# Kernel tuning notes

Hardware: AMD Instinct MI355X
Metric: run time of the kernel (lower is better)

## Reference

```python
import jax, jax.numpy as jnp
import numpy as np

HEADS = 16
SEGS = 8


def _rotate_half(x):
    x1, x2 = jnp.split(x, 2, axis=-1)
    return jnp.concatenate([-x2, x1], axis=-1)


def _split_heads(t, h):
    b, n, dim = t.shape
    d = dim // h
    return t.reshape(b, n, h, d).transpose(0, 2, 1, 3).reshape(b * h, n, d)


def _merge_heads(t, b, h):
    c, n, d = t.shape
    return t.reshape(b, h, n, d).transpose(0, 2, 1, 3).reshape(b, n, h * d)


def setup_inputs() -> dict:
    key = jax.random.key(0)
    ks = jax.random.split(key, 5)
    b, n, dim = 2, 4096, 1024
    x = jax.random.normal(ks[0], (b, n, dim), dtype=jnp.float32)
    w = lambda k: jax.random.normal(k, (dim, dim), dtype=jnp.float32) * 0.02
    return {
        'x': x,
        'Wq': w(ks[1]),
        'Wkv': w(ks[2]),
        'Wo': w(ks[3]),
        'bo': jnp.zeros((dim,), jnp.float32),
        'Wo0': w(ks[4]),
        'bo0': jnp.zeros((dim,), jnp.float32),
    }


def reference(x, Wq, Wkv, Wo, bo, Wo0, bo0):
    b, n, dim = x.shape
    h = HEADS
    d = dim // h
    s = SEGS
    m = n // s  # segment_len
    mask_value = -jnp.finfo(x.dtype).max

    q = _split_heads(x @ Wq, h)    # (b*h, n, d)
    kv = _split_heads(x @ Wkv, h)  # (b*h, n, d)  (serves as both keys and values)

    # rotary embedding (layer_num == 0 branch)
    inv_freq = 1.0 / (10000.0 ** (jnp.arange(0, d, 2, dtype=jnp.float32) / d))
    freqs = jnp.arange(n, dtype=jnp.float32)[:, None] * inv_freq[None, :]  # (n, d/2)
    rot = jnp.concatenate([freqs, freqs], axis=-1)[None]  # (1, n, d)
    cos, sin = jnp.cos(rot), jnp.sin(rot)
    q = q * cos + _rotate_half(q) * sin
    kv = kv * cos + _rotate_half(kv) * sin

    q = q * (d ** -0.5)

    qs = q.reshape(-1, s, m, d)   # (c, s, m, d)
    kvs = kv.reshape(-1, s, m, d)

    # overlapping windows: segment t paired with segment t+1 as kv context
    kvs_ccs = jnp.concatenate([kvs[:, :-1], kvs[:, 1:]], axis=2)  # (c, s-1, 2m, d)
    qs_ccs = qs[:, 1:]                                            # (c, s-1, m, d)

    # NOTE: original computes lkv = LayerNorm(kvs_ccs) but never uses it (dead code) -> omitted.

    lsim = jnp.einsum('csmd,csnd->csmn', qs_ccs, kvs_ccs)  # (c, s-1, m, 2m)
    causal = jnp.triu(jnp.ones((m, m), dtype=bool), 1)
    # causal mask only applied to second half of keys (the own segment t+1)
    lsim = jnp.concatenate(
        [lsim[..., :m], jnp.where(causal, mask_value, lsim[..., m:])], axis=-1)

    attn0 = jnp.einsum('csmd,csnd->csmn', qs[:, :1], kvs[:, :1])  # (c, 1, m, m)
    attn0 = jnp.where(causal, mask_value, attn0)

    attn0 = jax.nn.softmax(attn0, axis=-1)
    attn1 = jax.nn.softmax(lsim, axis=-1)

    out0 = jnp.einsum('csij,csjd->csid', attn0, kvs[:, :1]).reshape(-1, m, d)
    out1 = jnp.einsum('csij,csjd->csid', attn1, kvs_ccs).reshape(-1, (s - 1) * m, d)

    out0 = _merge_heads(out0, b, h) @ Wo0 + bo0  # (b, m, dim)
    out1 = _merge_heads(out1, b, h) @ Wo + bo    # (b, (s-1)*m, dim)
    return jnp.concatenate([out0, out1], axis=1)  # (b, n, dim)
```

## Files before the change

kernel.cpp:

```cpp
#include <hip/hip_runtime.h>
#include <hip/hip_bf16.h>
#include <float.h>

using bf16 = __hip_bfloat16;
typedef __attribute__((ext_vector_type(8))) short bf16x8;
typedef __attribute__((ext_vector_type(4))) float f32x4;
typedef __attribute__((ext_vector_type(16))) float f32x16;

#define DIM   1024
#define NSEQ  4096
#define BATCH 2
#define NH    16
#define HD    64
#define NSEG  8
#define MSEG  512
#define ROWS  (BATCH*NSEQ)
#define NC    (BATCH*NH)
#define QSCALE (0.125f * 1.44269504f)

__device__ __forceinline__ float fast_exp2(float x) {
    float r;
    asm volatile("v_exp_f32 %0, %1" : "=v"(r) : "v"(x));
    return r;
}

__device__ __forceinline__ void gload16(const bf16* g, bf16* l) {
    __builtin_amdgcn_global_load_lds((const __attribute__((address_space(1))) unsigned int*)g,
                                     (__attribute__((address_space(3))) unsigned int*)l, 16, 0, 0);
}

__global__ void k_prep(const float* __restrict__ x, bf16* __restrict__ Xb,
                       const float* __restrict__ Wq, const float* __restrict__ Wkv,
                       const float* __restrict__ Wo, const float* __restrict__ Wo0,
                       bf16* __restrict__ WqT, bf16* __restrict__ WkvT,
                       bf16* __restrict__ WoT, bf16* __restrict__ Wo0T,
                       float* __restrict__ cosT, float* __restrict__ sinT) {
    __shared__ float tile[32][33];
    int b = blockIdx.x, tid = threadIdx.x;
    if (b < 8192) {
        int i = (b * 256 + tid) * 4;
        float4 v = *(const float4*)&x[i];
        union { bf16 h[4]; uint2 u; } p;
        p.h[0] = __float2bfloat16(v.x);
        p.h[1] = __float2bfloat16(v.y);
        p.h[2] = __float2bfloat16(v.z);
        p.h[3] = __float2bfloat16(v.w);
        *(uint2*)&Xb[i] = p.u;
    } else if (b < 12288) {
        int zz = (b - 8192) >> 10;
        int bb = (b - 8192) & 1023;
        int bxt = (bb & 31) * 32, byt = (bb >> 5) * 32;
        const float* W = (zz == 0) ? Wq : (zz == 1) ? Wkv : (zz == 2) ? Wo : Wo0;
        bf16* Wt = (zz == 0) ? WqT : (zz == 1) ? WkvT : (zz == 2) ? WoT : Wo0T;
        int tx = tid & 31, ty = tid >> 5;
        for (int ii = ty; ii < 32; ii += 8)
            tile[ii][tx] = W[(size_t)(byt + ii) * DIM + bxt + tx];
        __syncthreads();
        for (int ii = ty; ii < 32; ii += 8)
            Wt[(size_t)(bxt + ii) * DIM + byt + tx] = __float2bfloat16(tile[tx][ii]);
    } else {
        int idx = (b - 12288) * 256 + tid;
        int t = idx >> 5, ii = idx & 31;
        float freq = 1.0f / powf(10000.0f, (float)(2 * ii) * (1.0f / 64.0f));
        float a = (float)t * freq;
        cosT[idx] = cosf(a);
        sinT[idx] = sinf(a);
    }
}

__launch_bounds__(256, 3)
__global__ void k_gemm_qkv(const bf16* __restrict__ A, const bf16* __restrict__ Bq,
                           const bf16* __restrict__ Bkv, const float* __restrict__ cosT,
                           const float* __restrict__ sinT, bf16* __restrict__ Qb,
                           bf16* __restrict__ KVf) {
    __shared__ alignas(16) bf16 SH[24576];
    bf16* AsB = SH;
    bf16* BsB = SH + 12288;
    const int K = DIM;
    int tid = threadIdx.x;
    int lane = tid & 63, wave = tid >> 6;
    int hi = lane >> 5, lq = lane & 31;
    int wr = (wave >> 1) * 64, wc = (wave & 1) * 64;
    int id = blockIdx.x;
    int xcd = id & 7, rank = id >> 3;
    int by = xcd * 8 + (rank >> 4);
    int bxx = rank & 15;
    int m0 = by * 128;
    bool isQ = (bxx < 8);
    const bf16* Bt = isQ ? Bq : Bkv;
    int n0 = (bxx & 7) * 128;
    int row = lane & 15, kk = (lane >> 4) * 8;
    int kkA = kk ^ (((lane >> 1) & 3) << 3);
    int ch0 = wave * 128 + lane, ch1 = ch0 + 64;
    int r0 = ch0 >> 2, c0e = (ch0 & 3) * 8;
    int r1 = ch1 >> 2, c1e = (ch1 & 3) * 8;
    int c0s = c0e ^ (((r0 >> 1) & 3) << 3);
    int c1s = c1e ^ (((r1 >> 1) & 3) << 3);
    f32x4 acc[4][4] = {};

    auto stage = [&](int k0, int b) {
        gload16(&A[(size_t)(m0 + r0) * K + k0 + c0s], &AsB[b * 4096 + wave * 1024]);
        gload16(&A[(size_t)(m0 + r1) * K + k0 + c1s], &AsB[b * 4096 + wave * 1024 + 512]);
        gload16(&Bt[(size_t)(n0 + r0) * K + k0 + c0s], &BsB[b * 4096 + wave * 1024]);
        gload16(&Bt[(size_t)(n0 + r1) * K + k0 + c1s], &BsB[b * 4096 + wave * 1024 + 512]);
    };
    stage(0, 0);
    stage(32, 1);
    asm volatile("s_waitcnt vmcnt(4)" ::: "memory");
    __builtin_amdgcn_s_barrier();
    __builtin_amdgcn_sched_barrier(0);
    int cur = 0;
    for (int k = 0; k < 32; ++k) {
        if (k + 2 < 32) {
            int nb = cur + 2; if (nb >= 3) nb -= 3;
            stage(k * 32 + 64, nb);
        }
        bf16x8 af[4], bfr[4];
#pragma unroll
        for (int mt = 0; mt < 4; ++mt) af[mt] = *(const bf16x8*)&AsB[cur * 4096 + (wr + mt * 16 + row) * 32 + kkA];
#pragma unroll
        for (int nt = 0; nt < 4; ++nt) bfr[nt] = *(const bf16x8*)&BsB[cur * 4096 + (wc + nt * 16 + row) * 32 + kkA];
#pragma unroll
        for (int mt = 0; mt < 4; ++mt)
#pragma unroll
            for (int nt = 0; nt < 4; ++nt)
                acc[mt][nt] = __builtin_amdgcn_mfma_f32_16x16x32_bf16(af[mt], bfr[nt], acc[mt][nt], 0, 0, 0);
        if (k + 1 < 32) {
            if (k + 2 < 32) asm volatile("s_waitcnt vmcnt(4)" ::: "memory");
            else            asm volatile("s_waitcnt vmcnt(0)" ::: "memory");
            __builtin_amdgcn_s_barrier();
            __builtin_amdgcn_sched_barrier(0);
        }
        cur = cur + 1; if (cur == 3) cur = 0;
    }
    __syncthreads();
    bf16* Tw = SH + wave * (64 * 72);
    int orow = (lane >> 4) * 4, ocol = lane & 15;
    int head_g = (n0 + wc) >> 6;
    float sc = isQ ? QSCALE : 1.0f;
    int bidx = (m0 + wr) >> 12;
    int tbase = (m0 + wr) & (NSEQ - 1);
    int cch = bidx * NH + head_g;
#pragma unroll
    for (int mt = 0; mt < 4; ++mt) {
#pragma unroll
        for (int i = 0; i < 4; ++i) {
            int rl = mt * 16 + orow + i;
            int t = tbase + rl;
#pragma unroll
            for (int nt = 0; nt < 2; ++nt) {
                int e = nt * 16 + ocol;
                float x1 = acc[mt][nt][i], x2 = acc[mt][nt + 2][i];
                float cv = cosT[t * 32 + e], sv = sinT[t * 32 + e];
                Tw[rl * 72 + e]      = __float2bfloat16((x1 * cv - x2 * sv) * sc);
                Tw[rl * 72 + e + 32] = __float2bfloat16((x2 * cv + x1 * sv) * sc);
            }
        }
    }
    if (isQ) {
        int rsub = lane >> 3, dg = (lane & 7) * 8;
        size_t qbase = ((size_t)cch * NSEQ + tbase) * HD;
#pragma unroll
        for (int rr = 0; rr < 8; ++rr) {
            int rl = rr * 8 + rsub;
            *(uint4*)&Qb[qbase + (size_t)rl * HD + dg] = *(const uint4*)&Tw[rl * 72 + dg];
        }
    } else {
        size_t kvfbase = ((size_t)cch * 128 + (tbase >> 5)) * 4096;
#pragma unroll
        for (int st = 0; st < 2; ++st) {
            size_t tb = kvfbase + (size_t)st * 4096;
#pragma unroll
            for (int f = 0; f < 4; ++f)
                *(uint4*)&KVf[tb + f * 512 + lane * 8] =
                    *(const uint4*)&Tw[(st * 32 + lq) * 72 + f * 16 + hi * 8];
#pragma unroll
            for (int m = 0; m < 4; ++m) {
                int d0 = (m >> 1) * 32, sb = m & 1;
                union { bf16 h[8]; uint4 u; } pk;
#pragma unroll
                for (int j = 0; j < 8; ++j)
                    pk.h[j] = Tw[(st * 32 + sb * 16 + hi * 8 + j) * 72 + d0 + lq];
                *(uint4*)&KVf[tb + (size_t)(4 + m) * 512 + lane * 8] = pk.u;
            }
        }
    }
}

__launch_bounds__(256, 4)
__global__ void k_gemm_out(const bf16* __restrict__ A, const bf16* __restrict__ Bt0,
                           const bf16* __restrict__ Bt1, const float* __restrict__ bias0,
                           const float* __restrict__ bias1, float* __restrict__ C) {
    __shared__ alignas(16) bf16 As[3][128 * 32];
    __shared__ alignas(16) bf16 Bs[3][64 * 32];
    const int K = DIM;
    int tid = threadIdx.x;
    int lane = tid & 63, wave = tid >> 6;
    int wr = (wave >> 1) * 64, wc = (wave & 1) * 32;
    int id = blockIdx.x;
    int xcd = id & 7, rank = id >> 3;
    int by = xcd * 8 + (rank >> 4);
    int bx = rank & 15;
    int m0 = by * 128, n0 = bx * 64;
    bool first = (m0 & (NSEQ - 1)) < MSEG;
    const bf16* Bt = first ? Bt0 : Bt1;
    const float* bias = first ? bias0 : bias1;
    int row = lane & 15, kk = (lane >> 4) * 8;
    int kkA = kk ^ (((lane >> 1) & 3) << 3);
    int ch0 = wave * 128 + lane, ch1 = ch0 + 64;
    int r0 = ch0 >> 2, c0e = (ch0 & 3) * 8;
    int r1 = ch1 >> 2, c1e = (ch1 & 3) * 8;
    int c0s = c0e ^ (((r0 >> 1) & 3) << 3);
    int c1s = c1e ^ (((r1 >> 1) & 3) << 3);
    int cb = wave * 64 + lane;
    int rb = cb >> 2, cbe = (cb & 3) * 8;
    int cbs = cbe ^ (((rb >> 1) & 3) << 3);
    f32x4 acc[4][2] = {};

    auto stage = [&](int k0, int b) {
        gload16(&A[(size_t)(m0 + r0) * K + k0 + c0s], &As[b][wave * 1024]);
        gload16(&A[(size_t)(m0 + r1) * K + k0 + c1s], &As[b][wave * 1024 + 512]);
        gload16(&Bt[(size_t)(n0 + rb) * K + k0 + cbs], &Bs[b][wave * 512]);
    };
    stage(0, 0);
    stage(32, 1);
    asm volatile("s_waitcnt vmcnt(3)" ::: "memory");
    __builtin_amdgcn_s_barrier();
    __builtin_amdgcn_sched_barrier(0);
    int cur = 0;
    for (int k = 0; k < 32; ++k) {
        if (k + 2 < 32) {
            int nb = cur + 2; if (nb >= 3) nb -= 3;
            stage(k * 32 + 64, nb);
        }
        bf16x8 af[4], bfr[2];
#pragma unroll
        for (int mt = 0; mt < 4; ++mt) af[mt] = *(const bf16x8*)&As[cur][(wr + mt * 16 + row) * 32 + kkA];
#pragma unroll
        for (int nt = 0; nt < 2; ++nt) bfr[nt] = *(const bf16x8*)&Bs[cur][(wc + nt * 16 + row) * 32 + kkA];
#pragma unroll
        for (int mt = 0; mt < 4; ++mt)
#pragma unroll
            for (int nt = 0; nt < 2; ++nt)
                acc[mt][nt] = __builtin_amdgcn_mfma_f32_16x16x32_bf16(af[mt], bfr[nt], acc[mt][nt], 0, 0, 0);
        if (k + 1 < 32) {
            if (k + 2 < 32) asm volatile("s_waitcnt vmcnt(3)" ::: "memory");
            else            asm volatile("s_waitcnt vmcnt(0)" ::: "memory");
            __builtin_amdgcn_s_barrier();
            __builtin_amdgcn_sched_barrier(0);
        }
        cur = cur + 1; if (cur == 3) cur = 0;
    }
    int orow = (lane >> 4) * 4, ocol = lane & 15;
#pragma unroll
    for (int mt = 0; mt < 4; ++mt)
#pragma unroll
        for (int nt = 0; nt < 2; ++nt) {
            float bv = bias[n0 + wc + nt * 16 + ocol];
#pragma unroll
            for (int i = 0; i < 4; ++i)
                C[(size_t)(m0 + wr + mt * 16 + orow + i) * DIM + n0 + wc + nt * 16 + ocol] = acc[mt][nt][i] + bv;
        }
}

__launch_bounds__(256, 4)
__global__ void k_attn(const bf16* __restrict__ Qb, const bf16* __restrict__ KVf,
                       bf16* __restrict__ Ob) {
    __shared__ float Osh[2][32][68];
    __shared__ float Msh[4][32];
    __shared__ float Lsh[4][32];
    int lane = threadIdx.x & 63, wave = threadIdx.x >> 6;
    int hi = lane >> 5, lq = lane & 31;
    int half = wave >> 1, qsel = wave & 1;
    int id = blockIdx.x;
    int xcd = id & 7, rank = id >> 3;
    int c = xcd * 4 + (rank & 3);
    int hr = rank >> 2;
    int j, seg;
    if (hr < 56) { j = 7 - hr / 7; seg = 1 + hr % 7; }
    else         { seg = 0; j = 63 - hr; }
    int qb = 2 * j + qsel;
    int i0 = qb * 32;
    int bidx = c >> 4, head = c & 15;
    int tq = seg * MSEG + i0 + lq;
    const bf16* qptr = &Qb[((size_t)c * NSEQ + tq) * HD + hi * 8];
    bf16x8 qf[4];
#pragma unroll
    for (int dc = 0; dc < 4; ++dc) qf[dc] = *(const bf16x8*)&qptr[dc * 16];
    f32x16 o0 = {}, o1 = {};
    float mrun = -FLT_MAX, lrun = 0.f;
    int kvbase = (seg == 0) ? 0 : (seg - 1) * MSEG;
    int cstart = (seg == 0) ? 0 : MSEG;
    int nT = (cstart + i0 + 32) >> 5;
    int hmid = (nT + 1) >> 1;
    int h0 = half ? hmid : 0;
    int h1 = half ? nT : hmid;

    const bf16* fb = &KVf[((size_t)c * 128 + (kvbase >> 5)) * 4096 + lane * 8];

    for (int it = h0; it < h1; ++it) {
        int c0 = it * 32;
        const bf16* pt = fb + (size_t)it * 4096;
        bf16x8 kf0 = *(const bf16x8*)&pt[0];
        bf16x8 kf1 = *(const bf16x8*)&pt[512];
        bf16x8 kf2 = *(const bf16x8*)&pt[1024];
        bf16x8 kf3 = *(const bf16x8*)&pt[1536];
        f32x16 s = {};
        __builtin_amdgcn_s_setprio(1);
        s = __builtin_amdgcn_mfma_f32_32x32x16_bf16(kf0, qf[0], s, 0, 0, 0);
        s = __builtin_amdgcn_mfma_f32_32x32x16_bf16(kf1, qf[1], s, 0, 0, 0);
        s = __builtin_amdgcn_mfma_f32_32x32x16_bf16(kf2, qf[2], s, 0, 0, 0);
        s = __builtin_amdgcn_mfma_f32_32x32x16_bf16(kf3, qf[3], s, 0, 0, 0);
        __builtin_amdgcn_s_setprio(0);
        bf16x8 vf0 = *(const bf16x8*)&pt[2048];
        bf16x8 vf1 = *(const bf16x8*)&pt[2560];
        bf16x8 vf2 = *(const bf16x8*)&pt[3072];
        bf16x8 vf3 = *(const bf16x8*)&pt[3584];
        if (c0 + 31 >= cstart && c0 + 31 - cstart > i0) {
#pragma unroll
            for (int r = 0; r < 16; ++r) {
                int kvg = c0 + ((r & 3) + 8 * (r >> 2) + 4 * hi);
                if (kvg >= cstart && kvg - cstart > i0 + lq) s[r] = -FLT_MAX;
            }
        }
        float m8[8], m4[4];
#pragma unroll
        for (int r = 0; r < 8; ++r) m8[r] = fmaxf(s[2 * r], s[2 * r + 1]);
#pragma unroll
        for (int r = 0; r < 4; ++r) m4[r] = fmaxf(m8[2 * r], m8[2 * r + 1]);
        float vmax = fmaxf(fmaxf(m4[0], m4[1]), fmaxf(m4[2], m4[3]));
        vmax = fmaxf(vmax, __shfl_xor(vmax, 32));
        if (__any(vmax > mrun + 11.5f)) {
            float nm = fmaxf(mrun, vmax);
            float al = fast_exp2(mrun - nm);
#pragma unroll
            for (int r = 0; r < 16; ++r) { o0[r] *= al; o1[r] *= al; }
            lrun *= al;
            mrun = nm;
        }
        float p[16];
#pragma unroll
        for (int r = 0; r < 16; ++r) p[r] = fast_exp2(s[r] - mrun);
        float a8[8], a4[4];
#pragma unroll
        for (int r = 0; r < 8; ++r) a8[r] = p[2 * r] + p[2 * r + 1];
#pragma unroll
        for (int r = 0; r < 4; ++r) a4[r] = a8[2 * r] + a8[2 * r + 1];
        lrun += (a4[0] + a4[1]) + (a4[2] + a4[3]);
        unsigned pk[8];
#pragma unroll
        for (int k = 0; k < 8; ++k) {
            union { bf16 h[2]; unsigned u; } cv;
            cv.h[0] = __float2bfloat16(p[2 * k]);
            cv.h[1] = __float2bfloat16(p[2 * k + 1]);
            pk[k] = cv.u;
        }
        unsigned u0 = hi ? pk[0] : pk[2];
        unsigned u1 = hi ? pk[1] : pk[3];
        unsigned u2 = hi ? pk[4] : pk[6];
        unsigned u3 = hi ? pk[5] : pk[7];
        unsigned w0 = (unsigned)__shfl_xor((int)u0, 32);
        unsigned w1 = (unsigned)__shfl_xor((int)u1, 32);
        unsigned w2 = (unsigned)__shfl_xor((int)u2, 32);
        unsigned w3 = (unsigned)__shfl_xor((int)u3, 32);
        union { unsigned u[4]; bf16x8 v; } b0, b1;
        b0.u[0] = hi ? w0 : pk[0];
        b0.u[1] = hi ? w1 : pk[1];
        b0.u[2] = hi ? pk[2] : w0;
        b0.u[3] = hi ? pk[3] : w1;
        b1.u[0] = hi ? w2 : pk[4];
        b1.u[1] = hi ? w3 : pk[5];
        b1.u[2] = hi ? pk[6] : w2;
        b1.u[3] = hi ? pk[7] : w3;
        __builtin_amdgcn_s_setprio(1);
        o0 = __builtin_amdgcn_mfma_f32_32x32x16_bf16(vf0, b0.v, o0, 0, 0, 0);
        o1 = __builtin_amdgcn_mfma_f32_32x32x16_bf16(vf2, b0.v, o1, 0, 0, 0);
        o0 = __builtin_amdgcn_mfma_f32_32x32x16_bf16(vf1, b1.v, o0, 0, 0, 0);
        o1 = __builtin_amdgcn_mfma_f32_32x32x16_bf16(vf3, b1.v, o1, 0, 0, 0);
        __builtin_amdgcn_s_setprio(0);
    }
    lrun += __shfl_xor(lrun, 32);
    if (lane < 32) { Msh[wave][lq] = mrun; Lsh[wave][lq] = lrun; }
    __syncthreads();
    float mp = Msh[wave ^ 2][lq];
    float M = fmaxf(mrun, mp);
    float scl = fast_exp2(mrun - M);
    if (half == 0) {
#pragma unroll
        for (int r = 0; r < 16; ++r) {
            int d = (r & 3) + 8 * (r >> 2) + 4 * hi;
            Osh[qsel][lq][d]      = o0[r] * scl;
            Osh[qsel][lq][d + 32] = o1[r] * scl;
        }
    }
    __syncthreads();
    if (half == 1) {
        float lt = lrun * scl + Lsh[wave ^ 2][lq] * fast_exp2(mp - M);
        float inv = 1.0f / lt;
#pragma unroll
        for (int r = 0; r < 16; ++r) {
            int d = (r & 3) + 8 * (r >> 2) + 4 * hi;
            o0[r] = o0[r] * scl + Osh[qsel][lq][d];
            o1[r] = o1[r] * scl + Osh[qsel][lq][d + 32];
        }
        size_t obase = ((size_t)bidx * NSEQ + tq) * DIM + head * HD;
#pragma unroll
        for (int dt = 0; dt < 2; ++dt)
#pragma unroll
            for (int a = 0; a < 4; ++a) {
                union { bf16 h[4]; uint2 u; } pkd;
                const f32x16& ov = dt ? o1 : o0;
#pragma unroll
                for (int i = 0; i < 4; ++i) pkd.h[i] = __float2bfloat16(ov[4 * a + i] * inv);
                *(uint2*)&Ob[obase + dt * 32 + 8 * a + 4 * hi] = pkd.u;
            }
    }
}

extern "C" void kernel_launch(void* const* d_in, const int* in_sizes, int n_in,
                              void* d_out, int out_size, void* d_ws, size_t ws_size,
                              hipStream_t stream) {
    const float* x   = (const float*)d_in[0];
    const float* Wq  = (const float*)d_in[1];
    const float* Wkv = (const float*)d_in[2];
    const float* Wo  = (const float*)d_in[3];
    const float* bo  = (const float*)d_in[4];
    const float* Wo0 = (const float*)d_in[5];
    const float* bo0 = (const float*)d_in[6];
    float* out = (float*)d_out;

    char* ws = (char*)d_ws;
    size_t off = 0;
    auto alloc = [&](size_t bytes) { void* p = ws + off; off += (bytes + 255) & ~(size_t)255; return p; };
    float* cosT = (float*)alloc((size_t)NSEQ * 32 * 4);
    float* sinT = (float*)alloc((size_t)NSEQ * 32 * 4);
    bf16* Xb    = (bf16*)alloc((size_t)ROWS * DIM * 2);
    bf16* WqT   = (bf16*)alloc((size_t)DIM * DIM * 2);
    bf16* WkvT  = (bf16*)alloc((size_t)DIM * DIM * 2);
    bf16* WoT   = (bf16*)alloc((size_t)DIM * DIM * 2);
    bf16* Wo0T  = (bf16*)alloc((size_t)DIM * DIM * 2);
    bf16* Qb    = (bf16*)alloc((size_t)NC * NSEQ * HD * 2);
    bf16* KVf   = (bf16*)alloc((size_t)NC * 128 * 4096 * 2);
    bf16* Ob    = (bf16*)alloc((size_t)ROWS * DIM * 2);

    hipLaunchKernelGGL(k_prep, dim3(12800), dim3(256), 0, stream,
                       x, Xb, Wq, Wkv, Wo, Wo0, WqT, WkvT, WoT, Wo0T, cosT, sinT);

    hipLaunchKernelGGL(k_gemm_qkv, dim3(1024), dim3(256), 0, stream, Xb, WqT, WkvT, cosT, sinT, Qb, KVf);

    hipLaunchKernelGGL(k_attn, dim3(2048), dim3(256), 0, stream, Qb, KVf, Ob);

    hipLaunchKernelGGL(k_gemm_out, dim3(1024), dim3(256), 0, stream, Ob, Wo0T, WoT, bo0, bo, out);
}
```

Measured before the change: 138.3 us.

## Fuse Q and KV projections per block to share A-tile loads

Each GEMM block now computes both the Q and the KV output tiles for the same row range. It loads the A (activation) tile once and multiplies it against both weight matrices, with two accumulator sets. The grid is halved, the LDS staging buffer grows to hold both B tiles, and the launch bound drops from 3 to 2 blocks per CU to fit the doubled accumulators. This removes the redundant re-reading of X, at the cost of lower occupancy and higher register pressure in the epilogue.

```diff
diff --git a/kernel.cpp b/kernel.cpp
--- a/kernel.cpp
+++ b/kernel.cpp
@@ -68,12 +68,12 @@
     }
 }
 
-__launch_bounds__(256, 3)
+__launch_bounds__(256, 2)
 __global__ void k_gemm_qkv(const bf16* __restrict__ A, const bf16* __restrict__ Bq,
                            const bf16* __restrict__ Bkv, const float* __restrict__ cosT,
                            const float* __restrict__ sinT, bf16* __restrict__ Qb,
                            bf16* __restrict__ KVf) {
-    __shared__ alignas(16) bf16 SH[24576];
+    __shared__ alignas(16) bf16 SH[36864];
     bf16* AsB = SH;
     bf16* BsB = SH + 12288;
     const int K = DIM;
@@ -83,12 +83,9 @@
     int wr = (wave >> 1) * 64, wc = (wave & 1) * 64;
     int id = blockIdx.x;
     int xcd = id & 7, rank = id >> 3;
-    int by = xcd * 8 + (rank >> 4);
-    int bxx = rank & 15;
+    int by = xcd * 8 + (rank >> 3);
+    int n0 = (rank & 7) * 128;
     int m0 = by * 128;
-    bool isQ = (bxx < 8);
-    const bf16* Bt = isQ ? Bq : Bkv;
-    int n0 = (bxx & 7) * 128;
     int row = lane & 15, kk = (lane >> 4) * 8;
     int kkA = kk ^ (((lane >> 1) & 3) << 3);
     int ch0 = wave * 128 + lane, ch1 = ch0 + 64;
@@ -96,17 +93,20 @@
     int r1 = ch1 >> 2, c1e = (ch1 & 3) * 8;
     int c0s = c0e ^ (((r0 >> 1) & 3) << 3);
     int c1s = c1e ^ (((r1 >> 1) & 3) << 3);
-    f32x4 acc[4][4] = {};
+    f32x4 accQ[4][4] = {};
+    f32x4 accK[4][4] = {};
 
     auto stage = [&](int k0, int b) {
         gload16(&A[(size_t)(m0 + r0) * K + k0 + c0s], &AsB[b * 4096 + wave * 1024]);
         gload16(&A[(size_t)(m0 + r1) * K + k0 + c1s], &AsB[b * 4096 + wave * 1024 + 512]);
-        gload16(&Bt[(size_t)(n0 + r0) * K + k0 + c0s], &BsB[b * 4096 + wave * 1024]);
-        gload16(&Bt[(size_t)(n0 + r1) * K + k0 + c1s], &BsB[b * 4096 + wave * 1024 + 512]);
+        gload16(&Bq[(size_t)(n0 + r0) * K + k0 + c0s], &BsB[b * 8192 + wave * 1024]);
+        gload16(&Bq[(size_t)(n0 + r1) * K + k0 + c1s], &BsB[b * 8192 + wave * 1024 + 512]);
+        gload16(&Bkv[(size_t)(n0 + r0) * K + k0 + c0s], &BsB[b * 8192 + 4096 + wave * 1024]);
+        gload16(&Bkv[(size_t)(n0 + r1) * K + k0 + c1s], &BsB[b * 8192 + 4096 + wave * 1024 + 512]);
     };
     stage(0, 0);
     stage(32, 1);
-    asm volatile("s_waitcnt vmcnt(4)" ::: "memory");
+    asm volatile("s_waitcnt vmcnt(6)" ::: "memory");
     __builtin_amdgcn_s_barrier();
     __builtin_amdgcn_sched_barrier(0);
     int cur = 0;
@@ -115,18 +115,22 @@
             int nb = cur + 2; if (nb >= 3) nb -= 3;
             stage(k * 32 + 64, nb);
         }
-        bf16x8 af[4], bfr[4];
+        bf16x8 af[4], bq[4], bk[4];
 #pragma unroll
         for (int mt = 0; mt < 4; ++mt) af[mt] = *(const bf16x8*)&AsB[cur * 4096 + (wr + mt * 16 + row) * 32 + kkA];
 #pragma unroll
-        for (int nt = 0; nt < 4; ++nt) bfr[nt] = *(const bf16x8*)&BsB[cur * 4096 + (wc + nt * 16 + row) * 32 + kkA];
+        for (int nt = 0; nt < 4; ++nt) bq[nt] = *(const bf16x8*)&BsB[cur * 8192 + (wc + nt * 16 + row) * 32 + kkA];
+#pragma unroll
+        for (int nt = 0; nt < 4; ++nt) bk[nt] = *(const bf16x8*)&BsB[cur * 8192 + 4096 + (wc + nt * 16 + row) * 32 + kkA];
 #pragma unroll
         for (int mt = 0; mt < 4; ++mt)
 #pragma unroll
-            for (int nt = 0; nt < 4; ++nt)
-                acc[mt][nt] = __builtin_amdgcn_mfma_f32_16x16x32_bf16(af[mt], bfr[nt], acc[mt][nt], 0, 0, 0);
+            for (int nt = 0; nt < 4; ++nt) {
+                accQ[mt][nt] = __builtin_amdgcn_mfma_f32_16x16x32_bf16(af[mt], bq[nt], accQ[mt][nt], 0, 0, 0);
+                accK[mt][nt] = __builtin_amdgcn_mfma_f32_16x16x32_bf16(af[mt], bk[nt], accK[mt][nt], 0, 0, 0);
+            }
         if (k + 1 < 32) {
-            if (k + 2 < 32) asm volatile("s_waitcnt vmcnt(4)" ::: "memory");
+            if (k + 2 < 32) asm volatile("s_waitcnt vmcnt(6)" ::: "memory");
             else            asm volatile("s_waitcnt vmcnt(0)" ::: "memory");
             __builtin_amdgcn_s_barrier();
             __builtin_amdgcn_sched_barrier(0);
@@ -137,7 +141,6 @@
     bf16* Tw = SH + wave * (64 * 72);
     int orow = (lane >> 4) * 4, ocol = lane & 15;
     int head_g = (n0 + wc) >> 6;
-    float sc = isQ ? QSCALE : 1.0f;
     int bidx = (m0 + wr) >> 12;
     int tbase = (m0 + wr) & (NSEQ - 1);
     int cch = bidx * NH + head_g;
@@ -150,14 +153,14 @@
 #pragma unroll
             for (int nt = 0; nt < 2; ++nt) {
                 int e = nt * 16 + ocol;
-                float x1 = acc[mt][nt][i], x2 = acc[mt][nt + 2][i];
+                float x1 = accQ[mt][nt][i], x2 = accQ[mt][nt + 2][i];
                 float cv = cosT[t * 32 + e], sv = sinT[t * 32 + e];
-                Tw[rl * 72 + e]      = __float2bfloat16((x1 * cv - x2 * sv) * sc);
-                Tw[rl * 72 + e + 32] = __float2bfloat16((x2 * cv + x1 * sv) * sc);
-            }
-        }
-    }
-    if (isQ) {
+                Tw[rl * 72 + e]      = __float2bfloat16((x1 * cv - x2 * sv) * QSCALE);
+                Tw[rl * 72 + e + 32] = __float2bfloat16((x2 * cv + x1 * sv) * QSCALE);
+            }
+        }
+    }
+    {
         int rsub = lane >> 3, dg = (lane & 7) * 8;
         size_t qbase = ((size_t)cch * NSEQ + tbase) * HD;
 #pragma unroll
@@ -165,7 +168,24 @@
             int rl = rr * 8 + rsub;
             *(uint4*)&Qb[qbase + (size_t)rl * HD + dg] = *(const uint4*)&Tw[rl * 72 + dg];
         }
-    } else {
+    }
+#pragma unroll
+    for (int mt = 0; mt < 4; ++mt) {
+#pragma unroll
+        for (int i = 0; i < 4; ++i) {
+            int rl = mt * 16 + orow + i;
+            int t = tbase + rl;
+#pragma unroll
+            for (int nt = 0; nt < 2; ++nt) {
+                int e = nt * 16 + ocol;
+                float x1 = accK[mt][nt][i], x2 = accK[mt][nt + 2][i];
+                float cv = cosT[t * 32 + e], sv = sinT[t * 32 + e];
+                Tw[rl * 72 + e]      = __float2bfloat16(x1 * cv - x2 * sv);
+                Tw[rl * 72 + e + 32] = __float2bfloat16(x2 * cv + x1 * sv);
+            }
+        }
+    }
+    {
         size_t kvfbase = ((size_t)cch * 128 + (tbase >> 5)) * 4096;
 #pragma unroll
         for (int st = 0; st < 2; ++st) {
@@ -446,7 +466,7 @@
     hipLaunchKernelGGL(k_prep, dim3(12800), dim3(256), 0, stream,
                        x, Xb, Wq, Wkv, Wo, Wo0, WqT, WkvT, WoT, Wo0T, cosT, sinT);
 
-    hipLaunchKernelGGL(k_gemm_qkv, dim3(1024), dim3(256), 0, stream, Xb, WqT, WkvT, cosT, sinT, Qb, KVf);
+    hipLaunchKernelGGL(k_gemm_qkv, dim3(512), dim3(256), 0, stream, Xb, WqT, WkvT, cosT, sinT, Qb, KVf);
 
     hipLaunchKernelGGL(k_attn, dim3(2048), dim3(256), 0, stream, Qb, KVf, Ob);
 
```

Result: faster. 133.4 us, median of 3 (-3.6%).
